# Kernel tuning notes

Measured on AMD Instinct MI355X. Metric: run time of the kernel, lower is better.

The kernel has to match this reference:

```python
import jax, jax.numpy as jnp
import numpy as np

V, D, H, L, B, T = 32000, 1024, 1024, 4, 32, 128
PAD_ID = 0


def setup_inputs() -> dict:
    key = jax.random.key(0)
    ks = jax.random.split(key, 12)
    s = lambda fan: 1.0 / np.sqrt(fan)
    dec_input = jax.random.randint(ks[0], (B, T), 0, V)
    h0 = jax.random.normal(ks[1], (L, B, H), jnp.float32)
    c0 = jax.random.normal(ks[2], (L, B, H), jnp.float32)
    emb = jax.random.normal(ks[3], (V, D), jnp.float32) * 0.02
    emb = emb.at[PAD_ID].set(0.0)
    # all layers have input size H (layer0 input = embedding_dim = H)
    W_ih = jax.random.uniform(ks[4], (L, 4 * H, H), jnp.float32, -s(H), s(H))
    W_hh = jax.random.uniform(ks[5], (L, 4 * H, H), jnp.float32, -s(H), s(H))
    b_ih = jax.random.uniform(ks[6], (L, 4 * H), jnp.float32, -s(H), s(H))
    b_hh = jax.random.uniform(ks[7], (L, 4 * H), jnp.float32, -s(H), s(H))
    cls_W = jax.random.uniform(ks[8], (V, H), jnp.float32, -s(H), s(H))
    cls_b = jax.random.uniform(ks[9], (V,), jnp.float32, -s(H), s(H))
    return {"dec_input": dec_input, "h0": h0, "c0": c0, "emb": emb,
            "W_ih": W_ih, "W_hh": W_hh, "b_ih": b_ih, "b_hh": b_hh,
            "cls_W": cls_W, "cls_b": cls_b}


def _lstm_stack_step(carry, x_t, W_ih, W_hh, b_ih, b_hh):
    # carry: (h [L,B,H], c [L,B,H]); x_t: [B,H]
    h, c = carry
    inp = x_t
    hs, cs = [], []
    n_layers = W_ih.shape[0]
    for l in range(n_layers):
        gates = inp @ W_ih[l].T + h[l] @ W_hh[l].T + b_ih[l] + b_hh[l]
        i_g, f_g, g_g, o_g = jnp.split(gates, 4, axis=-1)
        c_new = jax.nn.sigmoid(f_g) * c[l] + jax.nn.sigmoid(i_g) * jnp.tanh(g_g)
        h_new = jax.nn.sigmoid(o_g) * jnp.tanh(c_new)
        inp = h_new + inp  # residual connection (dropout p=0)
        hs.append(h_new)
        cs.append(c_new)
    return (jnp.stack(hs, 0), jnp.stack(cs, 0)), inp


def reference(dec_input, h0, c0, emb, W_ih, W_hh, b_ih, b_hh, cls_W, cls_b):
    embedded = emb[dec_input]                 # [B,T,D]
    xs = jnp.swapaxes(embedded, 0, 1)         # [T,B,D]

    def step(carry, x_t):
        return _lstm_stack_step(carry, x_t, W_ih, W_hh, b_ih, b_hh)

    (hT, cT), outs = jax.lax.scan(step, (h0, c0), xs)  # outs: [T,B,H]
    outputs = jnp.swapaxes(outs, 0, 1)         # [B,T,H]
    logits = outputs @ cls_W.T + cls_b         # [B,T,V]
    return logits, (hT, cT)
```

## Files before the change

### kernel.cpp

```cpp
#include <hip/hip_runtime.h>
#include <stdint.h>

#define LAYERS 4
#define BATCH  32
#define SEQT   128
#define HID    1024
#define VOCAB  32000

typedef __attribute__((ext_vector_type(8))) short short8;
typedef __attribute__((ext_vector_type(8))) __bf16 bf16x8;
typedef __attribute__((ext_vector_type(4))) float floatx4;

#define CLS_OFF  0ul
#define X_OFF    65536000ul
#define RES_OFF  73924608ul
#define HBT_OFF  107479040ul
#define CF_OFF   141295616ul
#define SYNC_OFF 141819904ul

#define LOGITS_N 131072000ul
#define BH (BATCH * HID)

__device__ __forceinline__ unsigned short f2bf(float f) {
  union { float f; unsigned u; } v; v.f = f;
  unsigned r = v.u + 0x7FFF + ((v.u >> 16) & 1);
  return (unsigned short)(r >> 16);
}
__device__ __forceinline__ float bf2f(unsigned short b) {
  union { unsigned u; float f; } v; v.u = ((unsigned)b) << 16;
  return v.f;
}
__device__ __forceinline__ floatx4 mfma16(short8 a, short8 b, floatx4 c) {
  return __builtin_amdgcn_mfma_f32_16x16x32_bf16(
      __builtin_bit_cast(bf16x8, a), __builtin_bit_cast(bf16x8, b), c, 0, 0, 0);
}
__device__ __forceinline__ short8 cvt8(float4 a, float4 b) {
  short8 r;
  r[0] = (short)f2bf(a.x); r[1] = (short)f2bf(a.y);
  r[2] = (short)f2bf(a.z); r[3] = (short)f2bf(a.w);
  r[4] = (short)f2bf(b.x); r[5] = (short)f2bf(b.y);
  r[6] = (short)f2bf(b.z); r[7] = (short)f2bf(b.w);
  return r;
}


__global__ void k_convert(const float* __restrict__ clsw, unsigned short* __restrict__ oC) {
  const long long NC4 = 8192000LL;
  for (long long i = (long long)blockIdx.x * blockDim.x + threadIdx.x; i < NC4;
       i += (long long)gridDim.x * blockDim.x) {
    float4 v = *(const float4*)(clsw + (i << 2));
    ushort4 o; o.x = f2bf(v.x); o.y = f2bf(v.y); o.z = f2bf(v.z); o.w = f2bf(v.w);
    *(ushort4*)(oC + (i << 2)) = o;
  }
}

__global__ void k_embed(const int* __restrict__ tok, const float* __restrict__ emb,
                        unsigned short* __restrict__ X) {
  const int bt = blockIdx.x;
  const int t = bt >> 5, b = bt & 31;
  const int v = tok[b * SEQT + t];
  const float4* src = (const float4*)(emb + (size_t)v * HID);
  ushort4* dst = (ushort4*)(X + (size_t)bt * HID);
  const int i = threadIdx.x;
  float4 f = src[i];
  ushort4 o; o.x = f2bf(f.x); o.y = f2bf(f.y); o.z = f2bf(f.z); o.w = f2bf(f.w);
  dst[i] = o;
}

__global__ void k_init(const float* __restrict__ h0, const float* __restrict__ c0,
                       unsigned short* __restrict__ HBT, float* __restrict__ CF,
                       unsigned* __restrict__ sync) {
  const int i = blockIdx.x * blockDim.x + threadIdx.x;
  if (i < 4096) sync[i] = 0u;
  if (i < LAYERS * BATCH * HID) {
    HBT[i] = f2bf(h0[i]);
    CF[i] = c0[i];
  }
}


__global__ __launch_bounds__(512, 2) void k_lstm(
    const float* __restrict__ Wih, const float* __restrict__ Whh,
    const float* __restrict__ bih, const float* __restrict__ bhh,
    const unsigned short* __restrict__ X, unsigned short* __restrict__ RES,
    unsigned short* __restrict__ HBT, const float* __restrict__ CF,
    float* __restrict__ out, unsigned* __restrict__ syncp) {
  const int p = blockIdx.x;
  const int l = (p & 7) >> 1;
  const int jj = ((p >> 3) << 1) | (p & 1);
  const int j0 = jj << 4;
  const int tid = threadIdx.x;
  const int q = tid >> 6;
  const int lane = tid & 63;
  const int lo = lane & 15, hi = lane >> 4;
  const int u = tid & 15, b = tid >> 4;

  __shared__ float red[8][32][66];
  __shared__ unsigned mbx, mbh;

  if (tid == 0) { mbx = 0u; mbh = 0u; }

  (void)__hip_atomic_load(syncp + 2048, __ATOMIC_ACQUIRE, __HIP_MEMORY_SCOPE_AGENT);

  const unsigned* fx = syncp + (((l - 1) & 3) * 64 + lane) * 4;
  const unsigned* fh = syncp + (l * 64 + lane) * 4;
  unsigned* fown = syncp + (l * 64 + jj) * 4;

  short8 wx[4][4], wh[4][4];
  {
    const size_t lb = (size_t)l * 4096;
#pragma unroll
    for (int ct = 0; ct < 4; ++ct) {
#pragma unroll
      for (int ks = 0; ks < 4; ++ks) {
        const size_t off = (lb + (size_t)(ct * 1024 + j0 + lo)) * HID
                         + (size_t)q * 128 + ks * 32 + hi * 8;
        float4 a0 = *(const float4*)(Wih + off);
        float4 a1 = *(const float4*)(Wih + off + 4);
        wx[ct][ks] = cvt8(a0, a1);
        float4 b0 = *(const float4*)(Whh + off);
        float4 b1 = *(const float4*)(Whh + off + 4);
        wh[ct][ks] = cvt8(b0, b1);
      }
    }
  }
  float bias_g[4];
#pragma unroll
  for (int g = 0; g < 4; ++g)
    bias_g[g] = bih[l * 4096 + g * 1024 + j0 + u] + bhh[l * 4096 + g * 1024 + j0 + u];
  float c_reg = CF[(size_t)l * BH + (size_t)b * HID + j0 + u];

  __syncthreads();

  for (int t = 0; t < SEQT; ++t) {
    if (q == 0) {
      if (l > 0) {
        for (;;) {
          int ok = (__hip_atomic_load(fx, __ATOMIC_RELAXED, __HIP_MEMORY_SCOPE_AGENT)
                    >= (unsigned)(t + 1));
          if (__all(ok)) break;
          __builtin_amdgcn_s_sleep(1);
        }
      }
      __hip_atomic_store(&mbx, (unsigned)(t + 1),
                         __ATOMIC_RELAXED, __HIP_MEMORY_SCOPE_WORKGROUP);
    } else {
      while (__hip_atomic_load(&mbx, __ATOMIC_RELAXED, __HIP_MEMORY_SCOPE_WORKGROUP)
             < (unsigned)(t + 1))
        __builtin_amdgcn_s_sleep(1);
    }

    const unsigned short* xsrc = (l == 0)
        ? (X + (size_t)t * BH)
        : (RES + ((size_t)(l - 1) * SEQT + t) * BH);

    const unsigned short* px0 = xsrc + (size_t)lo * HID + q * 128 + hi * 8;
    const unsigned short* px1 = px0 + 16 * HID;
    const unsigned short* pxr = xsrc + (size_t)b * HID + j0 + u;

    short8 x0a, x0b, x0c, x0d, x1a, x1b, x1c, x1d;
    unsigned xres;
    asm volatile(
      "global_load_dwordx4 %0, %9,  off\n\t"
      "global_load_dwordx4 %1, %9,  off offset:64\n\t"
      "global_load_dwordx4 %2, %9,  off offset:128\n\t"
      "global_load_dwordx4 %3, %9,  off offset:192\n\t"
      "global_load_dwordx4 %4, %10, off\n\t"
      "global_load_dwordx4 %5, %10, off offset:64\n\t"
      "global_load_dwordx4 %6, %10, off offset:128\n\t"
      "global_load_dwordx4 %7, %10, off offset:192\n\t"
      "global_load_ushort  %8, %11, off\n\t"
      "s_waitcnt vmcnt(0)"
      : "=&v"(x0a), "=&v"(x0b), "=&v"(x0c), "=&v"(x0d),
        "=&v"(x1a), "=&v"(x1b), "=&v"(x1c), "=&v"(x1d), "=&v"(xres)
      : "v"(px0), "v"(px1), "v"(pxr)
      : "memory");

    floatx4 acc[4][2];
#pragma unroll
    for (int ct = 0; ct < 4; ++ct) { acc[ct][0] = {0,0,0,0}; acc[ct][1] = {0,0,0,0}; }
#pragma unroll
    for (int ct = 0; ct < 4; ++ct) {
      acc[ct][0] = mfma16(x0a, wx[ct][0], acc[ct][0]);
      acc[ct][1] = mfma16(x1a, wx[ct][0], acc[ct][1]);
      acc[ct][0] = mfma16(x0b, wx[ct][1], acc[ct][0]);
      acc[ct][1] = mfma16(x1b, wx[ct][1], acc[ct][1]);
      acc[ct][0] = mfma16(x0c, wx[ct][2], acc[ct][0]);
      acc[ct][1] = mfma16(x1c, wx[ct][2], acc[ct][1]);
      acc[ct][0] = mfma16(x0d, wx[ct][3], acc[ct][0]);
      acc[ct][1] = mfma16(x1d, wx[ct][3], acc[ct][1]);
    }

    if (q == 0) {
      if (t > 0) {
        for (;;) {
          int ok = (__hip_atomic_load(fh, __ATOMIC_RELAXED, __HIP_MEMORY_SCOPE_AGENT)
                    >= (unsigned)t);
          if (__all(ok)) break;
          __builtin_amdgcn_s_sleep(1);
        }
      }
      __hip_atomic_store(&mbh, (unsigned)(t + 1),
                         __ATOMIC_RELAXED, __HIP_MEMORY_SCOPE_WORKGROUP);
    } else {
      while (__hip_atomic_load(&mbh, __ATOMIC_RELAXED, __HIP_MEMORY_SCOPE_WORKGROUP)
             < (unsigned)(t + 1))
        __builtin_amdgcn_s_sleep(1);
    }

    const unsigned short* hsrc = HBT + ((size_t)t * LAYERS + l) * BH;
    const unsigned short* ph0 = hsrc + (size_t)lo * HID + q * 128 + hi * 8;
    const unsigned short* ph1 = ph0 + 16 * HID;

    short8 h0a, h0b, h0c, h0d, h1a, h1b, h1c, h1d;
    asm volatile(
      "global_load_dwordx4 %0, %8, off\n\t"
      "global_load_dwordx4 %1, %8, off offset:64\n\t"
      "global_load_dwordx4 %2, %8, off offset:128\n\t"
      "global_load_dwordx4 %3, %8, off offset:192\n\t"
      "global_load_dwordx4 %4, %9, off\n\t"
      "global_load_dwordx4 %5, %9, off offset:64\n\t"
      "global_load_dwordx4 %6, %9, off offset:128\n\t"
      "global_load_dwordx4 %7, %9, off offset:192\n\t"
      "s_waitcnt vmcnt(0)"
      : "=&v"(h0a), "=&v"(h0b), "=&v"(h0c), "=&v"(h0d),
        "=&v"(h1a), "=&v"(h1b), "=&v"(h1c), "=&v"(h1d)
      : "v"(ph0), "v"(ph1)
      : "memory");

#pragma unroll
    for (int ct = 0; ct < 4; ++ct) {
      acc[ct][0] = mfma16(h0a, wh[ct][0], acc[ct][0]);
      acc[ct][1] = mfma16(h1a, wh[ct][0], acc[ct][1]);
      acc[ct][0] = mfma16(h0b, wh[ct][1], acc[ct][0]);
      acc[ct][1] = mfma16(h1b, wh[ct][1], acc[ct][1]);
      acc[ct][0] = mfma16(h0c, wh[ct][2], acc[ct][0]);
      acc[ct][1] = mfma16(h1c, wh[ct][2], acc[ct][1]);
      acc[ct][0] = mfma16(h0d, wh[ct][3], acc[ct][0]);
      acc[ct][1] = mfma16(h1d, wh[ct][3], acc[ct][1]);
    }

#pragma unroll
    for (int ct = 0; ct < 4; ++ct)
#pragma unroll
      for (int rt = 0; rt < 2; ++rt)
#pragma unroll
        for (int r = 0; r < 4; ++r)
          red[q][rt * 16 + hi * 4 + r][ct * 16 + lo] = acc[ct][rt][r];
    __syncthreads();

    float gacc[4] = {0.f, 0.f, 0.f, 0.f};
#pragma unroll
    for (int qq = 0; qq < 8; ++qq)
#pragma unroll
      for (int g = 0; g < 4; ++g)
        gacc[g] += red[qq][b][g * 16 + u];

    const float ig = gacc[0] + bias_g[0];
    const float fg = gacc[1] + bias_g[1];
    const float gg = gacc[2] + bias_g[2];
    const float og = gacc[3] + bias_g[3];
    const float si = 1.f / (1.f + __expf(-ig));
    const float sf = 1.f / (1.f + __expf(-fg));
    const float so = 1.f / (1.f + __expf(-og));
    const float tg = 1.f - 2.f / (__expf(2.f * gg) + 1.f);
    const float cn = sf * c_reg + si * tg;
    const float hn = so * (1.f - 2.f / (__expf(2.f * cn) + 1.f));
    c_reg = cn;

    const float xval = bf2f((unsigned short)xres);
    const unsigned hbf = f2bf(hn);
    const unsigned rbf = f2bf(hn + xval);
    const unsigned hpk = hbf | (((unsigned)__shfl_xor((int)hbf, 1)) << 16);
    const unsigned rpk = rbf | (((unsigned)__shfl_xor((int)rbf, 1)) << 16);

    unsigned short* HBw = HBT + ((size_t)(t + 1) * LAYERS + l) * BH;
    unsigned short* RESw = RES + ((size_t)l * SEQT + t) * BH;
    const size_t hidx = (size_t)b * HID + j0 + u;
    if (!(tid & 1)) {
      __hip_atomic_store((unsigned*)(HBw + hidx), hpk,
                         __ATOMIC_RELAXED, __HIP_MEMORY_SCOPE_AGENT);
      __hip_atomic_store((unsigned*)(RESw + hidx), rpk,
                         __ATOMIC_RELAXED, __HIP_MEMORY_SCOPE_AGENT);
    }
    if (t == SEQT - 1) {
      out[LOGITS_N + (size_t)l * BH + hidx] = hn;
      out[LOGITS_N + 131072ul + (size_t)l * BH + hidx] = cn;
    }

    asm volatile("s_waitcnt vmcnt(0)" ::: "memory");
    __syncthreads();
    if (tid == 0)
      __hip_atomic_store(fown, (unsigned)(t + 1),
                         __ATOMIC_RELAXED, __HIP_MEMORY_SCOPE_AGENT);
  }
}


__global__ __launch_bounds__(256, 2) void k_cls(
    const unsigned short* __restrict__ A, const unsigned short* __restrict__ Bw,
    const float* __restrict__ bias, float* __restrict__ out) {
  __shared__ unsigned short lA[128 * 64];
  __shared__ unsigned short lB[128 * 64];
  const int ntile = blockIdx.x >> 5;
  const int mtile = blockIdx.x & 31;
  const int m0 = mtile << 7, n0 = ntile << 7;
  const int tid = threadIdx.x;
  const int w = tid >> 6, lane = tid & 63, lo = lane & 15, hi = lane >> 4;
  const int mw = (w >> 1) << 6, nw = (w & 1) << 6;

  floatx4 acc[4][4];
#pragma unroll
  for (int i = 0; i < 4; ++i)
#pragma unroll
    for (int j = 0; j < 4; ++j) acc[i][j] = {0.f, 0.f, 0.f, 0.f};

  for (int k0 = 0; k0 < HID; k0 += 64) {
#pragma unroll
    for (int qq = 0; qq < 4; ++qq) {
      const int e = qq * 256 + tid;
      const int row = e >> 3, c8 = e & 7;
      const int ps = row * 64 + ((c8 ^ (row & 7)) << 3);
      *(short8*)(lA + ps) = *(const short8*)(A  + (size_t)(m0 + row) * HID + k0 + (c8 << 3));
      *(short8*)(lB + ps) = *(const short8*)(Bw + (size_t)(n0 + row) * HID + k0 + (c8 << 3));
    }
    __syncthreads();
#pragma unroll
    for (int kk = 0; kk < 2; ++kk) {
      short8 af[4], bfr[4];
#pragma unroll
      for (int x = 0; x < 4; ++x) {
        const int ra = mw + x * 16 + lo;
        af[x]  = *(const short8*)(lA + ra * 64 + ((((kk << 2) + hi) ^ (ra & 7)) << 3));
        const int rb = nw + x * 16 + lo;
        bfr[x] = *(const short8*)(lB + rb * 64 + ((((kk << 2) + hi) ^ (rb & 7)) << 3));
      }
#pragma unroll
      for (int mi = 0; mi < 4; ++mi)
#pragma unroll
        for (int ni = 0; ni < 4; ++ni)
          acc[mi][ni] = mfma16(af[mi], bfr[ni], acc[mi][ni]);
    }
    __syncthreads();
  }

#pragma unroll
  for (int mi = 0; mi < 4; ++mi) {
#pragma unroll
    for (int ni = 0; ni < 4; ++ni) {
      const int v = n0 + nw + ni * 16 + lo;
      const float bv = bias[v];
#pragma unroll
      for (int r = 0; r < 4; ++r) {
        const int ra = m0 + mw + mi * 16 + hi * 4 + r;
        const int orow = (ra & 31) * SEQT + (ra >> 5);
        out[(size_t)orow * VOCAB + v] = acc[mi][ni][r] + bv;
      }
    }
  }
}


extern "C" void kernel_launch(void* const* d_in, const int* in_sizes, int n_in,
                              void* d_out, int out_size, void* d_ws, size_t ws_size,
                              hipStream_t stream) {
  (void)in_sizes; (void)n_in; (void)out_size; (void)ws_size;
  const int*   tok  = (const int*)d_in[0];
  const float* h0   = (const float*)d_in[1];
  const float* c0   = (const float*)d_in[2];
  const float* emb  = (const float*)d_in[3];
  const float* wih  = (const float*)d_in[4];
  const float* whh  = (const float*)d_in[5];
  const float* bih  = (const float*)d_in[6];
  const float* bhh  = (const float*)d_in[7];
  const float* clsw = (const float*)d_in[8];
  const float* clsb = (const float*)d_in[9];
  float* out = (float*)d_out;
  char* ws = (char*)d_ws;

  unsigned short* Cls = (unsigned short*)(ws + CLS_OFF);
  unsigned short* X   = (unsigned short*)(ws + X_OFF);
  unsigned short* RES = (unsigned short*)(ws + RES_OFF);
  unsigned short* HBT = (unsigned short*)(ws + HBT_OFF);
  float*          CF  = (float*)(ws + CF_OFF);
  unsigned*       SY  = (unsigned*)(ws + SYNC_OFF);

  hipLaunchKernelGGL(k_convert, dim3(2048), dim3(256), 0, stream, clsw, Cls);
  hipLaunchKernelGGL(k_embed,   dim3(SEQT * BATCH), dim3(256), 0, stream, tok, emb, X);
  hipLaunchKernelGGL(k_init,    dim3(512), dim3(256), 0, stream, h0, c0, HBT, CF, SY);

  {
    const float* a0 = wih; const float* a1 = whh; const float* a2 = bih; const float* a3 = bhh;
    const unsigned short* a4 = X; unsigned short* a5 = RES; unsigned short* a6 = HBT;
    const float* a7 = CF; float* a8 = out; unsigned* a9 = SY;
    void* kargs[] = {&a0, &a1, &a2, &a3, &a4, &a5, &a6, &a7, &a8, &a9};
    hipLaunchCooperativeKernel((void*)k_lstm, dim3(256), dim3(512), kargs, 0, stream);
  }

  hipLaunchKernelGGL(k_cls, dim3(250 * 32), dim3(256), 0, stream,
                     RES + (size_t)3 * SEQT * BATCH * HID, Cls, clsb, out);
}
```

Measured before the change: 1.288 ms.

## Give each wave full-K gate tiles to remove the LDS cross-wave reduction

Reassigns work so each wave owns 4 hidden units times 4 gates across 16 batch rows over the full K=1024 dimension, holding 32 bf16 weight fragments per matrix in registers. The MFMA output then lines up directly with the i/f/g/o gates for one (batch, unit) pair. This removes the 8-way shared-memory reduction and its __syncthreads from the per-timestep critical path. In exchange, register pressure rises sharply, so launch bounds drop to one block per SIMD pair. Each wave also reads entire activation rows with plain loads instead of the inline-asm batched loads, and the sync flag stride is changed from 4 words to 1.

```diff
diff --git a/kernel.cpp b/kernel.cpp
--- a/kernel.cpp
+++ b/kernel.cpp
@@ -79,7 +79,7 @@
 }
 
 
-__global__ __launch_bounds__(512, 2) void k_lstm(
+__global__ __launch_bounds__(512, 1) void k_lstm(
     const float* __restrict__ Wih, const float* __restrict__ Whh,
     const float* __restrict__ bih, const float* __restrict__ bhh,
     const unsigned short* __restrict__ X, unsigned short* __restrict__ RES,
@@ -90,50 +90,49 @@
   const int jj = ((p >> 3) << 1) | (p & 1);
   const int j0 = jj << 4;
   const int tid = threadIdx.x;
-  const int q = tid >> 6;
+  const int w = tid >> 6;
+  const int ut = w >> 1;
+  const int rt = w & 1;
   const int lane = tid & 63;
   const int lo = lane & 15, hi = lane >> 4;
-  const int u = tid & 15, b = tid >> 4;
-
-  __shared__ float red[8][32][66];
+  const int unit = j0 + ut * 4 + hi;
+  const int bat  = rt * 16 + lo;
+
   __shared__ unsigned mbx, mbh;
-
   if (tid == 0) { mbx = 0u; mbh = 0u; }
 
   (void)__hip_atomic_load(syncp + 2048, __ATOMIC_ACQUIRE, __HIP_MEMORY_SCOPE_AGENT);
 
-  const unsigned* fx = syncp + (((l - 1) & 3) * 64 + lane) * 4;
-  const unsigned* fh = syncp + (l * 64 + lane) * 4;
-  unsigned* fown = syncp + (l * 64 + jj) * 4;
-
-  short8 wx[4][4], wh[4][4];
+  const unsigned* fx = syncp + ((l - 1) & 3) * 64 + lane;
+  const unsigned* fh = syncp + l * 64 + lane;
+  unsigned* fown = syncp + l * 64 + jj;
+
+  short8 wxr[32], whr[32];
   {
-    const size_t lb = (size_t)l * 4096;
-#pragma unroll
-    for (int ct = 0; ct < 4; ++ct) {
-#pragma unroll
-      for (int ks = 0; ks < 4; ++ks) {
-        const size_t off = (lb + (size_t)(ct * 1024 + j0 + lo)) * HID
-                         + (size_t)q * 128 + ks * 32 + hi * 8;
-        float4 a0 = *(const float4*)(Wih + off);
-        float4 a1 = *(const float4*)(Wih + off + 4);
-        wx[ct][ks] = cvt8(a0, a1);
-        float4 b0 = *(const float4*)(Whh + off);
-        float4 b1 = *(const float4*)(Whh + off + 4);
-        wh[ct][ks] = cvt8(b0, b1);
-      }
+    const size_t grow = (size_t)l * 4096 + (size_t)(lo & 3) * 1024
+                      + j0 + ut * 4 + (lo >> 2);
+    const float* pwx = Wih + grow * HID + hi * 8;
+    const float* pwh = Whh + grow * HID + hi * 8;
+#pragma unroll
+    for (int ks = 0; ks < 32; ++ks) {
+      float4 a0 = *(const float4*)(pwx + ks * 32);
+      float4 a1 = *(const float4*)(pwx + ks * 32 + 4);
+      wxr[ks] = cvt8(a0, a1);
+      float4 b0 = *(const float4*)(pwh + ks * 32);
+      float4 b1 = *(const float4*)(pwh + ks * 32 + 4);
+      whr[ks] = cvt8(b0, b1);
     }
   }
   float bias_g[4];
 #pragma unroll
   for (int g = 0; g < 4; ++g)
-    bias_g[g] = bih[l * 4096 + g * 1024 + j0 + u] + bhh[l * 4096 + g * 1024 + j0 + u];
-  float c_reg = CF[(size_t)l * BH + (size_t)b * HID + j0 + u];
+    bias_g[g] = bih[l * 4096 + g * 1024 + unit] + bhh[l * 4096 + g * 1024 + unit];
+  float c_reg = CF[(size_t)l * BH + (size_t)bat * HID + unit];
 
   __syncthreads();
 
   for (int t = 0; t < SEQT; ++t) {
-    if (q == 0) {
+    if (w == 0) {
       if (l > 0) {
         for (;;) {
           int ok = (__hip_atomic_load(fx, __ATOMIC_RELAXED, __HIP_MEMORY_SCOPE_AGENT)
@@ -153,45 +152,23 @@
     const unsigned short* xsrc = (l == 0)
         ? (X + (size_t)t * BH)
         : (RES + ((size_t)(l - 1) * SEQT + t) * BH);
-
-    const unsigned short* px0 = xsrc + (size_t)lo * HID + q * 128 + hi * 8;
-    const unsigned short* px1 = px0 + 16 * HID;
-    const unsigned short* pxr = xsrc + (size_t)b * HID + j0 + u;
-
-    short8 x0a, x0b, x0c, x0d, x1a, x1b, x1c, x1d;
-    unsigned xres;
-    asm volatile(
-      "global_load_dwordx4 %0, %9,  off\n\t"
-      "global_load_dwordx4 %1, %9,  off offset:64\n\t"
-      "global_load_dwordx4 %2, %9,  off offset:128\n\t"
-      "global_load_dwordx4 %3, %9,  off offset:192\n\t"
-      "global_load_dwordx4 %4, %10, off\n\t"
-      "global_load_dwordx4 %5, %10, off offset:64\n\t"
-      "global_load_dwordx4 %6, %10, off offset:128\n\t"
-      "global_load_dwordx4 %7, %10, off offset:192\n\t"
-      "global_load_ushort  %8, %11, off\n\t"
-      "s_waitcnt vmcnt(0)"
-      : "=&v"(x0a), "=&v"(x0b), "=&v"(x0c), "=&v"(x0d),
-        "=&v"(x1a), "=&v"(x1b), "=&v"(x1c), "=&v"(x1d), "=&v"(xres)
-      : "v"(px0), "v"(px1), "v"(pxr)
-      : "memory");
-
-    floatx4 acc[4][2];
-#pragma unroll
-    for (int ct = 0; ct < 4; ++ct) { acc[ct][0] = {0,0,0,0}; acc[ct][1] = {0,0,0,0}; }
-#pragma unroll
-    for (int ct = 0; ct < 4; ++ct) {
-      acc[ct][0] = mfma16(x0a, wx[ct][0], acc[ct][0]);
-      acc[ct][1] = mfma16(x1a, wx[ct][0], acc[ct][1]);
-      acc[ct][0] = mfma16(x0b, wx[ct][1], acc[ct][0]);
-      acc[ct][1] = mfma16(x1b, wx[ct][1], acc[ct][1]);
-      acc[ct][0] = mfma16(x0c, wx[ct][2], acc[ct][0]);
-      acc[ct][1] = mfma16(x1c, wx[ct][2], acc[ct][1]);
-      acc[ct][0] = mfma16(x0d, wx[ct][3], acc[ct][0]);
-      acc[ct][1] = mfma16(x1d, wx[ct][3], acc[ct][1]);
-    }
-
-    if (q == 0) {
+    const short8* xrow = (const short8*)xsrc + (size_t)bat * 128;
+    const float xval = bf2f(xsrc[(size_t)bat * HID + unit]);
+
+    floatx4 acc0 = {0.f, 0.f, 0.f, 0.f}, acc1 = {0.f, 0.f, 0.f, 0.f};
+#pragma unroll
+    for (int cph = 0; cph < 2; ++cph) {
+      short8 f[16];
+#pragma unroll
+      for (int i = 0; i < 16; ++i) f[i] = xrow[(cph * 16 + i) * 4 + hi];
+#pragma unroll
+      for (int i = 0; i < 16; i += 2) {
+        acc0 = mfma16(wxr[cph * 16 + i],     f[i],     acc0);
+        acc1 = mfma16(wxr[cph * 16 + i + 1], f[i + 1], acc1);
+      }
+    }
+
+    if (w == 0) {
       if (t > 0) {
         for (;;) {
           int ok = (__hip_atomic_load(fh, __ATOMIC_RELAXED, __HIP_MEMORY_SCOPE_AGENT)
@@ -208,53 +185,20 @@
         __builtin_amdgcn_s_sleep(1);
     }
 
-    const unsigned short* hsrc = HBT + ((size_t)t * LAYERS + l) * BH;
-    const unsigned short* ph0 = hsrc + (size_t)lo * HID + q * 128 + hi * 8;
-    const unsigned short* ph1 = ph0 + 16 * HID;
-
-    short8 h0a, h0b, h0c, h0d, h1a, h1b, h1c, h1d;
-    asm volatile(
-      "global_load_dwordx4 %0, %8, off\n\t"
-      "global_load_dwordx4 %1, %8, off offset:64\n\t"
-      "global_load_dwordx4 %2, %8, off offset:128\n\t"
-      "global_load_dwordx4 %3, %8, off offset:192\n\t"
-      "global_load_dwordx4 %4, %9, off\n\t"
-      "global_load_dwordx4 %5, %9, off offset:64\n\t"
-      "global_load_dwordx4 %6, %9, off offset:128\n\t"
-      "global_load_dwordx4 %7, %9, off offset:192\n\t"
-      "s_waitcnt vmcnt(0)"
-      : "=&v"(h0a), "=&v"(h0b), "=&v"(h0c), "=&v"(h0d),
-        "=&v"(h1a), "=&v"(h1b), "=&v"(h1c), "=&v"(h1d)
-      : "v"(ph0), "v"(ph1)
-      : "memory");
-
-#pragma unroll
-    for (int ct = 0; ct < 4; ++ct) {
-      acc[ct][0] = mfma16(h0a, wh[ct][0], acc[ct][0]);
-      acc[ct][1] = mfma16(h1a, wh[ct][0], acc[ct][1]);
-      acc[ct][0] = mfma16(h0b, wh[ct][1], acc[ct][0]);
-      acc[ct][1] = mfma16(h1b, wh[ct][1], acc[ct][1]);
-      acc[ct][0] = mfma16(h0c, wh[ct][2], acc[ct][0]);
-      acc[ct][1] = mfma16(h1c, wh[ct][2], acc[ct][1]);
-      acc[ct][0] = mfma16(h0d, wh[ct][3], acc[ct][0]);
-      acc[ct][1] = mfma16(h1d, wh[ct][3], acc[ct][1]);
-    }
-
-#pragma unroll
-    for (int ct = 0; ct < 4; ++ct)
-#pragma unroll
-      for (int rt = 0; rt < 2; ++rt)
-#pragma unroll
-        for (int r = 0; r < 4; ++r)
-          red[q][rt * 16 + hi * 4 + r][ct * 16 + lo] = acc[ct][rt][r];
-    __syncthreads();
-
-    float gacc[4] = {0.f, 0.f, 0.f, 0.f};
-#pragma unroll
-    for (int qq = 0; qq < 8; ++qq)
-#pragma unroll
-      for (int g = 0; g < 4; ++g)
-        gacc[g] += red[qq][b][g * 16 + u];
+    const short8* hrow = (const short8*)(HBT + ((size_t)t * LAYERS + l) * BH)
+                       + (size_t)bat * 128;
+#pragma unroll
+    for (int cph = 0; cph < 2; ++cph) {
+      short8 f[16];
+#pragma unroll
+      for (int i = 0; i < 16; ++i) f[i] = hrow[(cph * 16 + i) * 4 + hi];
+#pragma unroll
+      for (int i = 0; i < 16; i += 2) {
+        acc0 = mfma16(whr[cph * 16 + i],     f[i],     acc0);
+        acc1 = mfma16(whr[cph * 16 + i + 1], f[i + 1], acc1);
+      }
+    }
+    const floatx4 gacc = acc0 + acc1;
 
     const float ig = gacc[0] + bias_g[0];
     const float fg = gacc[1] + bias_g[1];
@@ -268,24 +212,23 @@
     const float hn = so * (1.f - 2.f / (__expf(2.f * cn) + 1.f));
     c_reg = cn;
 
-    const float xval = bf2f((unsigned short)xres);
     const unsigned hbf = f2bf(hn);
     const unsigned rbf = f2bf(hn + xval);
-    const unsigned hpk = hbf | (((unsigned)__shfl_xor((int)hbf, 1)) << 16);
-    const unsigned rpk = rbf | (((unsigned)__shfl_xor((int)rbf, 1)) << 16);
-
-    unsigned short* HBw = HBT + ((size_t)(t + 1) * LAYERS + l) * BH;
-    unsigned short* RESw = RES + ((size_t)l * SEQT + t) * BH;
-    const size_t hidx = (size_t)b * HID + j0 + u;
-    if (!(tid & 1)) {
-      __hip_atomic_store((unsigned*)(HBw + hidx), hpk,
+    const unsigned ho = (unsigned)__shfl_xor((int)hbf, 16);
+    const unsigned ro = (unsigned)__shfl_xor((int)rbf, 16);
+    if (!(hi & 1)) {
+      const size_t hidx = (size_t)bat * HID + unit;
+      unsigned short* HBw = HBT + ((size_t)(t + 1) * LAYERS + l) * BH;
+      unsigned short* RESw = RES + ((size_t)l * SEQT + t) * BH;
+      __hip_atomic_store((unsigned*)(HBw + hidx), hbf | (ho << 16),
                          __ATOMIC_RELAXED, __HIP_MEMORY_SCOPE_AGENT);
-      __hip_atomic_store((unsigned*)(RESw + hidx), rpk,
+      __hip_atomic_store((unsigned*)(RESw + hidx), rbf | (ro << 16),
                          __ATOMIC_RELAXED, __HIP_MEMORY_SCOPE_AGENT);
     }
     if (t == SEQT - 1) {
-      out[LOGITS_N + (size_t)l * BH + hidx] = hn;
-      out[LOGITS_N + 131072ul + (size_t)l * BH + hidx] = cn;
+      const size_t oidx = (size_t)l * BH + (size_t)bat * HID + unit;
+      out[LOGITS_N + oidx] = hn;
+      out[LOGITS_N + 131072ul + oidx] = cn;
     }
 
     asm volatile("s_waitcnt vmcnt(0)" ::: "memory");
```

After: 3.275 ms. +154.2%, slower.
